# Kernel tuning notes

Measured on AMD Instinct MI355X. Metric: run time of the kernel, lower is better.

Reference implementation:

```python
import jax, jax.numpy as jnp
import numpy as np

C = 512

def _xavier(key, shape, gain=1.0):
    fan_in, fan_out = shape[1], shape[0]
    a = gain * np.sqrt(6.0 / (fan_in + fan_out))
    return jax.random.uniform(key, shape, jnp.float32, -a, a)

def setup_inputs() -> dict:
    key = jax.random.key(0)
    ks = jax.random.split(key, 5)
    x = jax.random.normal(ks[0], (32, C, 32, 32), jnp.float32)
    # 1x1 conv weights as [out_ch, in_ch]; biases zero-init per module
    Wq = _xavier(ks[1], (C, C))
    Wk = _xavier(ks[2], (C, C))
    Wv = _xavier(ks[3], (C, C))
    Wo = _xavier(ks[4], (C, C), gain=1e-05)
    zeros = jnp.zeros((C,), jnp.float32)
    return {"x": x, "Wq": Wq, "bq": zeros, "Wk": Wk, "bk": zeros,
            "Wv": Wv, "bv": zeros, "Wo": Wo, "bo": zeros}

def _proj(x, W, b):
    # 1x1 conv: x [B,C,H,W], W [Cout,Cin] -> [B,Cout,H,W]
    return jnp.einsum('bchw,oc->bohw', x, W) + b[None, :, None, None]

def reference(x, Wq, bq, Wk, bk, Wv, bv, Wo, bo):
    B, Cc, H, W = x.shape
    q = _proj(x, Wq, bq).transpose(0, 2, 3, 1).reshape(B, H * W, Cc)  # [B,HW,C]
    k = _proj(x, Wk, bk).reshape(B, Cc, H * W)                        # [B,C,HW]
    v = _proj(x, Wv, bv).transpose(0, 2, 3, 1).reshape(B, H * W, Cc)  # [B,HW,C]
    w = jnp.einsum('bnc,bcm->bnm', q, k) * (Cc ** -0.5)               # [B,HW,HW]
    w = jax.nn.softmax(w, axis=-1)
    h = jnp.einsum('bnm,bmc->bnc', w, v)                              # [B,HW,C]
    h = h.reshape(B, H, W, Cc).transpose(0, 3, 1, 2)                  # [B,C,H,W]
    h = _proj(h, Wo, bo)
    return x + h
```

## Files before the change

### kernel.cpp

```cpp
#include <hip/hip_runtime.h>
#include <stdint.h>


#define CD 512
#define NSP 1024
#define SCALE_EXP2 0.06376339f
#define WO_SCALE 4194304.0f
#define WO_INV   2.384185791015625e-7f

using bf16x8 = __attribute__((ext_vector_type(8))) short;
using f32x4  = __attribute__((ext_vector_type(4))) float;
typedef long i64v;

__device__ __forceinline__ unsigned char f2f8(float f) {
    unsigned int r;
    asm("v_cvt_pk_fp8_f32 %0, %1, %1" : "=v"(r) : "v"(f));
    return (unsigned char)(r & 0xffu);
}
__device__ __forceinline__ unsigned int f4_to_f8x4(float a, float b, float c, float d) {
    unsigned int r = 0;
    asm("v_cvt_pk_fp8_f32 %0, %2, %3\n\t"
        "v_cvt_pk_fp8_f32 %0, %4, %5 op_sel:[0,0,1]"
        : "=v"(r) : "0"(r), "v"(a), "v"(b), "v"(c), "v"(d));
    return r;
}
__device__ __forceinline__ void gl_lds16(const void* g, void* l) {
    __builtin_amdgcn_global_load_lds(
        (const __attribute__((address_space(1))) void*)g,
        (__attribute__((address_space(3))) void*)l, 16, 0, 0);
}

__global__ __launch_bounds__(256) void cvt_all(
    const float* __restrict__ Wq, const float* __restrict__ Wk,
    const float* __restrict__ Wv, const float* __restrict__ Wo,
    const float* __restrict__ bq, const float* __restrict__ bk,
    unsigned char* __restrict__ w8, float* __restrict__ bqk)
{
    int idx = blockIdx.x * 256 + threadIdx.x;
    int which = idx >> 18, off = idx & 262143;
    const float* src = which == 0 ? Wq : which == 1 ? Wk : which == 2 ? Wv : Wo;
    float v = src[off] * (which == 3 ? WO_SCALE : 1.0f);
    w8[idx] = f2f8(v);
    if (idx < 1024) bqk[idx] = (idx < 512) ? bq[idx] : bk[idx - 512];
}

__global__ __launch_bounds__(256) void transpose_x(const float* __restrict__ x,
                                                   unsigned char* __restrict__ xt) {
    __shared__ float t[32][33];
    int b = blockIdx.z;
    int n0 = blockIdx.x * 32, c0 = blockIdx.y * 32;
    const float* xb = x + (size_t)b * CD * NSP;
    unsigned char* xtb = xt + (size_t)b * NSP * CD;
    int tx = threadIdx.x, ty = threadIdx.y;
    #pragma unroll
    for (int i = 0; i < 4; ++i)
        t[ty + i * 8][tx] = xb[(size_t)(c0 + ty + i * 8) * NSP + n0 + tx];
    __syncthreads();
    #pragma unroll
    for (int i = 0; i < 4; ++i)
        xtb[(size_t)(n0 + ty + i * 8) * CD + c0 + tx] = f2f8(t[tx][ty + i * 8]);
}

template<int BIAS_MODE, bool RESID, bool OUT_F32>
__global__ __launch_bounds__(256)
void gemm_bt8(const unsigned char* __restrict__ A,
              const unsigned char* __restrict__ B,
              void* __restrict__ Cv,
              const float* __restrict__ bias,
              const float* __restrict__ resid,
              int K, int lda, int ldb, int ldc,
              long sA, long sB, long sC, long sR, float alpha)
{
    __shared__ __align__(16) unsigned char As[2][128 * 64];
    __shared__ __align__(16) unsigned char Bs[2][128 * 64];

    const int z = blockIdx.z;
    const unsigned char* Ab = A + (size_t)z * sA + (size_t)blockIdx.y * 128 * lda;
    const unsigned char* Bb = B + (size_t)z * sB + (size_t)blockIdx.x * 128 * ldb;

    const int t = threadIdx.x;
    const int lane = t & 63;
    const int wave = t >> 6;
    const int wr = wave >> 1, wc = wave & 1;
    const int lr = lane & 15, lk = lane >> 4;

    f32x4 acc[4][4] = {};

    const int KT = K >> 6;
    auto stage = [&](int kt, int buf) {
        int k0 = kt << 6;
        #pragma unroll
        for (int i = 0; i < 2; ++i) {
            int rb = i * 64 + wave * 16;
            int row = rb + (lane >> 2);
            int src = (lane & 3) ^ ((row >> 1) & 3);
            gl_lds16(Ab + (size_t)row * lda + k0 + src * 16, &As[buf][rb * 64]);
            gl_lds16(Bb + (size_t)row * ldb + k0 + src * 16, &Bs[buf][rb * 64]);
        }
    };
    stage(0, 0);
    for (int kt = 0; kt < KT; ++kt) {
        int cur = kt & 1;
        if (kt + 1 < KT) {
            stage(kt + 1, cur ^ 1);
            asm volatile("s_waitcnt vmcnt(4)" ::: "memory");
        } else {
            asm volatile("s_waitcnt vmcnt(0)" ::: "memory");
        }
        __builtin_amdgcn_s_barrier();
        const unsigned char* Ac = &As[cur][0];
        const unsigned char* Bc = &Bs[cur][0];
        #pragma unroll
        for (int kk = 0; kk < 2; ++kk) {
            int c16 = kk * 2 + (lk >> 1);
            int half = (lk & 1) * 8;
            i64v af[4], bfr[4];
            #pragma unroll
            for (int f = 0; f < 4; ++f) {
                int arow = wr * 64 + f * 16 + lr;
                af[f] = *(const i64v*)&Ac[arow * 64 + ((c16 ^ ((arow >> 1) & 3)) << 4) + half];
                int brow = wc * 64 + f * 16 + lr;
                bfr[f] = *(const i64v*)&Bc[brow * 64 + ((c16 ^ ((brow >> 1) & 3)) << 4) + half];
            }
            #pragma unroll
            for (int fm = 0; fm < 4; ++fm)
                #pragma unroll
                for (int fn = 0; fn < 4; ++fn)
                    acc[fm][fn] = __builtin_amdgcn_mfma_f32_16x16x32_fp8_fp8(
                        af[fm], bfr[fn], acc[fm][fn], 0, 0, 0);
        }
        asm volatile("s_waitcnt lgkmcnt(0)" ::: "memory");
        __builtin_amdgcn_s_barrier();
    }

    const int m0 = blockIdx.y * 128;
    const int n0 = blockIdx.x * 128;
    unsigned char* C8 = (unsigned char*)Cv + (size_t)z * sC;
    float* Cf = (float*)Cv + (size_t)z * sC;
    const float* rp = RESID ? resid + (size_t)z * sR : nullptr;
    #pragma unroll
    for (int fm = 0; fm < 4; ++fm) {
        #pragma unroll
        for (int fn = 0; fn < 4; ++fn) {
            int col = n0 + wc * 64 + fn * 16 + lr;
            int rowb = m0 + wr * 64 + fm * 16 + lk * 4;
            #pragma unroll
            for (int j = 0; j < 4; ++j) {
                int row = rowb + j;
                float v = acc[fm][fn][j] * alpha;
                if (BIAS_MODE == 1) v += bias[col];
                if (BIAS_MODE == 2) v += bias[row];
                if (RESID) v += rp[(size_t)row * ldc + col];
                if (OUT_F32) Cf[(size_t)row * ldc + col] = v;
                else         C8[(size_t)row * ldc + col] = f2f8(v);
            }
        }
    }
}

__global__ __launch_bounds__(512, 2)
void flash_attn(const unsigned char* __restrict__ Q,
                const unsigned char* __restrict__ Kg,
                const unsigned char* __restrict__ Vg,
                unsigned char* __restrict__ H)
{
    __shared__ __align__(16) unsigned char Ks[2][64 * 512];
    __shared__ __align__(16) unsigned char Vs[2][512 * 64];
    __shared__ __align__(16) unsigned char Ps[2][128 * 72];
    __shared__ __align__(16) float Ls[2][128];
    __shared__ int flags[2];

    const int p = blockIdx.x;
    const int b  = ((p >> 6) << 3) + (p & 7);
    const int qt = (p >> 3) & 7;

    const int tid = threadIdx.x;
    const int w = tid >> 6, lane = tid & 63;
    const int lr = lane & 15, lk = lane >> 4;
    const int q0 = qt * 128 + w * 16;

    i64v qf[16];
    const unsigned char* qp = Q + ((size_t)b * NSP + q0 + lr) * 1024 + lk * 8;
    #pragma unroll
    for (int st = 0; st < 16; ++st) qf[st] = *(const i64v*)(qp + st * 32);

    f32x4 o[8][4] = {};
    float m = -3.0e38f, l = 0.f;

    const unsigned char* Kb = Kg + (size_t)b * NSP * 1024;
    const unsigned char* Vb = Vg + (size_t)b * CD * 1024;

    auto stageK = [&](int t, int buf) {
        int kv0 = t * 64;
        #pragma unroll
        for (int i = 0; i < 4; ++i) {
            int rb = i * 16 + w * 2;
            int row = rb + (lane >> 5);
            int src = (lane & 31) ^ (row & 7);
            gl_lds16(Kb + (size_t)(kv0 + row) * 1024 + src * 16, &Ks[buf][rb * 512]);
        }
    };
    auto stageV = [&](int t, int buf) {
        int kv0 = t * 64;
        #pragma unroll
        for (int i = 0; i < 4; ++i) {
            int cb = i * 128 + w * 16;
            int c = cb + (lane >> 2);
            int src = (lane & 3) ^ ((c >> 1) & 3);
            gl_lds16(Vb + (size_t)c * 1024 + kv0 + src * 16, &Vs[buf][cb * 64]);
        }
    };

    auto qksm = [&](int tau) {
        const int pb = tau & 1;
        const unsigned char* Kc = &Ks[pb][0];
        f32x4 s[4] = {};
        __builtin_amdgcn_s_setprio(1);
        #pragma unroll
        for (int st = 0; st < 16; ++st) {
            int c16 = st * 2 + (lk >> 1);
            int half = (lk & 1) * 8;
            #pragma unroll
            for (int kvf = 0; kvf < 4; ++kvf) {
                int row = kvf * 16 + lr;
                i64v kf = *(const i64v*)&Kc[row * 512 + ((c16 ^ (row & 7)) << 4) + half];
                s[kvf] = __builtin_amdgcn_mfma_f32_16x16x32_fp8_fp8(kf, qf[st], s[kvf], 0, 0, 0);
            }
        }
        __builtin_amdgcn_s_setprio(0);
        #pragma unroll
        for (int kvf = 0; kvf < 4; ++kvf)
            #pragma unroll
            for (int j = 0; j < 4; ++j) s[kvf][j] *= SCALE_EXP2;

        float pm = fmaxf(fmaxf(fmaxf(s[0][0], s[0][1]), fmaxf(s[0][2], s[0][3])),
                         fmaxf(fmaxf(s[1][0], s[1][1]), fmaxf(s[1][2], s[1][3])));
        pm = fmaxf(pm, fmaxf(fmaxf(fmaxf(s[2][0], s[2][1]), fmaxf(s[2][2], s[2][3])),
                             fmaxf(fmaxf(s[3][0], s[3][1]), fmaxf(s[3][2], s[3][3]))));
        pm = fmaxf(pm, __shfl_xor(pm, 16));
        pm = fmaxf(pm, __shfl_xor(pm, 32));
        bool ev = !__all(pm - m <= 8.0f);
        float mn = fmaxf(m, pm);
        float sc = ev ? exp2f(m - mn) : 1.0f;
        if (ev) { m = mn; l *= sc; }
        if (lk == 0) Ls[pb][w * 16 + lr] = sc;
        if (ev && lane == 0) flags[pb] = tau;

        float rs = 0.f;
        #pragma unroll
        for (int kvf = 0; kvf < 4; ++kvf)
            #pragma unroll
            for (int j = 0; j < 4; ++j) {
                s[kvf][j] = exp2f(s[kvf][j] - m);
                rs += s[kvf][j];
            }
        rs += __shfl_xor(rs, 16);
        rs += __shfl_xor(rs, 32);
        l += rs;

        #pragma unroll
        for (int kvf = 0; kvf < 4; ++kvf) {
            unsigned int pk = f4_to_f8x4(s[kvf][0], s[kvf][1], s[kvf][2], s[kvf][3]);
            *(unsigned int*)&Ps[pb][(w * 16 + lr) * 72 + kvf * 16 + lk * 4] = pk;
        }
    };

    if (tid == 0) { flags[0] = -1; flags[1] = -1; }
    stageK(0, 0); stageV(0, 0);
    asm volatile("s_waitcnt vmcnt(0) lgkmcnt(0)" ::: "memory");
    __builtin_amdgcn_s_barrier();
    stageK(1, 1);
    qksm(0);
    asm volatile("s_waitcnt vmcnt(0) lgkmcnt(0)" ::: "memory");
    __builtin_amdgcn_s_barrier();

    for (int t = 0; t < 16; ++t) {
        const int cur = t & 1;
        if (t < 14) stageK(t + 2, cur);
        if (t < 15) stageV(t + 1, cur ^ 1);

        if (flags[cur] == t) {
            #pragma unroll
            for (int qf2 = 0; qf2 < 8; ++qf2) {
                f32x4 scv = *(const f32x4*)&Ls[cur][qf2 * 16 + lk * 4];
                #pragma unroll
                for (int cf = 0; cf < 4; ++cf) {
                    o[qf2][cf][0] *= scv[0]; o[qf2][cf][1] *= scv[1];
                    o[qf2][cf][2] *= scv[2]; o[qf2][cf][3] *= scv[3];
                }
            }
        }
        const unsigned char* Vc = &Vs[cur][0];
        __builtin_amdgcn_s_setprio(1);
        #pragma unroll
        for (int ks = 0; ks < 2; ++ks) {
            int c16 = ks * 2 + (lk >> 1);
            int half = (lk & 1) * 8;
            i64v vfr[4];
            #pragma unroll
            for (int cf = 0; cf < 4; ++cf) {
                int c = w * 64 + cf * 16 + lr;
                vfr[cf] = *(const i64v*)&Vc[c * 64 + ((c16 ^ ((c >> 1) & 3)) << 4) + half];
            }
            #pragma unroll
            for (int qf2 = 0; qf2 < 8; ++qf2) {
                i64v pa = *(const i64v*)&Ps[cur][(qf2 * 16 + lr) * 72 + ks * 32 + lk * 8];
                #pragma unroll
                for (int cf = 0; cf < 4; ++cf)
                    o[qf2][cf] = __builtin_amdgcn_mfma_f32_16x16x32_fp8_fp8(
                        pa, vfr[cf], o[qf2][cf], 0, 0, 0);
            }
        }
        __builtin_amdgcn_s_setprio(0);

        if (t < 15) qksm(t + 1);

        asm volatile("s_waitcnt vmcnt(0) lgkmcnt(0)" ::: "memory");
        __builtin_amdgcn_s_barrier();
    }

    if (lk == 0) Ls[0][w * 16 + lr] = 1.0f / l;
    asm volatile("s_waitcnt lgkmcnt(0)" ::: "memory");
    __builtin_amdgcn_s_barrier();
    unsigned char* Hp = H + ((size_t)b * NSP + qt * 128) * CD + w * 64;
    #pragma unroll
    for (int qf2 = 0; qf2 < 8; ++qf2) {
        f32x4 li = *(const f32x4*)&Ls[0][qf2 * 16 + lk * 4];
        #pragma unroll
        for (int cf = 0; cf < 4; ++cf) {
            #pragma unroll
            for (int j = 0; j < 4; ++j)
                Hp[(size_t)(qf2 * 16 + lk * 4 + j) * CD + cf * 16 + lr] =
                    f2f8(o[qf2][cf][j] * li[j]);
        }
    }
}

extern "C" void kernel_launch(void* const* d_in, const int* in_sizes, int n_in,
                              void* d_out, int out_size, void* d_ws, size_t ws_size,
                              hipStream_t stream)
{
    const float* x  = (const float*)d_in[0];
    const float* Wq = (const float*)d_in[1];
    const float* bq = (const float*)d_in[2];
    const float* Wk = (const float*)d_in[3];
    const float* bk = (const float*)d_in[4];
    const float* Wv = (const float*)d_in[5];
    const float* bv = (const float*)d_in[6];
    const float* Wo = (const float*)d_in[7];
    const float* bo = (const float*)d_in[8];
    float* out = (float*)d_out;

    unsigned char* w = (unsigned char*)d_ws;
    unsigned char* W8  = w;
    float*         bqk = (float*)(w + 1048576);
    unsigned char* Xt8 = w + 1052672;
    unsigned char* QK8 = w + 17829888;
    unsigned char* Vc8 = w + 51384320;
    unsigned char* H8  = w + 68161536;

    cvt_all<<<4096, 256, 0, stream>>>(Wq, Wk, Wv, Wo, bq, bk, W8, bqk);
    transpose_x<<<dim3(32, 16, 32), dim3(32, 8), 0, stream>>>(x, Xt8);

    gemm_bt8<1, false, false><<<dim3(8, 256, 1), 256, 0, stream>>>(
        Xt8, W8, QK8, bqk, nullptr, 512, 512, 512, 1024, 0, 0, 0, 0, 1.0f);

    gemm_bt8<2, false, false><<<dim3(8, 4, 32), 256, 0, stream>>>(
        W8 + 524288, Xt8, Vc8, bv, nullptr, 512, 512, 512, 1024,
        0, 524288, 524288, 0, 1.0f);

    flash_attn<<<256, 512, 0, stream>>>(QK8, QK8 + 512, Vc8, H8);

    gemm_bt8<2, true, true><<<dim3(8, 4, 32), 256, 0, stream>>>(
        W8 + 786432, H8, out, bo, x, 512, 512, 512, 1024,
        0, 524288, 524288, 524288, WO_INV);
}
```

Baseline: 196.9 us.

## Interleave QK and PV MFMAs in flash attention; enlarge projection GEMM tiles

The flash attention loop now issues the PV MFMAs for tile t and the QK^T MFMAs for tile t+1 in one interleaved loop, followed by softmax. The aim is to overlap LDS fragment loads with MFMA work and shorten the dependency chain. The last iteration is peeled out. Separately, the QKV projection GEMMs move to a 256x128 tile with 4x8 fragments per wave, which improves operand reuse but raises register pressure and halves the block count.

```diff
diff --git a/kernel.cpp b/kernel.cpp
--- a/kernel.cpp
+++ b/kernel.cpp
@@ -8,7 +8,6 @@
 #define WO_SCALE 4194304.0f
 #define WO_INV   2.384185791015625e-7f
 
-using bf16x8 = __attribute__((ext_vector_type(8))) short;
 using f32x4  = __attribute__((ext_vector_type(4))) float;
 typedef long i64v;
 
@@ -61,21 +60,120 @@
         xtb[(size_t)(n0 + ty + i * 8) * CD + c0 + tx] = f2f8(t[tx][ty + i * 8]);
 }
 
-template<int BIAS_MODE, bool RESID, bool OUT_F32>
+template<int BIAS_MODE>
 __global__ __launch_bounds__(256)
-void gemm_bt8(const unsigned char* __restrict__ A,
-              const unsigned char* __restrict__ B,
-              void* __restrict__ Cv,
-              const float* __restrict__ bias,
-              const float* __restrict__ resid,
-              int K, int lda, int ldb, int ldc,
-              long sA, long sB, long sC, long sR, float alpha)
+void gemm_bt8_256(const unsigned char* __restrict__ A,
+                  const unsigned char* __restrict__ B,
+                  unsigned char* __restrict__ C8,
+                  const float* __restrict__ bias,
+                  int K, int lda, int ldb, int ldc,
+                  long sA, long sB, long sC)
+{
+    __shared__ __align__(16) unsigned char As[2][256 * 64];
+    __shared__ __align__(16) unsigned char Bs[2][128 * 64];
+
+    const int z = blockIdx.z;
+    const unsigned char* Ab = A + (size_t)z * sA + (size_t)blockIdx.y * 256 * lda;
+    const unsigned char* Bb = B + (size_t)z * sB + (size_t)blockIdx.x * 128 * ldb;
+
+    const int t = threadIdx.x;
+    const int lane = t & 63;
+    const int wave = t >> 6;
+    const int lr = lane & 15, lk = lane >> 4;
+
+    f32x4 acc[4][8] = {};
+
+    const int KT = K >> 6;
+    auto stage = [&](int kt, int buf) {
+        int k0 = kt << 6;
+        #pragma unroll
+        for (int i = 0; i < 4; ++i) {
+            int rb = i * 64 + wave * 16;
+            int row = rb + (lane >> 2);
+            int src = (lane & 3) ^ ((row >> 1) & 3);
+            gl_lds16(Ab + (size_t)row * lda + k0 + src * 16, &As[buf][rb * 64]);
+        }
+        #pragma unroll
+        for (int i = 0; i < 2; ++i) {
+            int rb = i * 64 + wave * 16;
+            int row = rb + (lane >> 2);
+            int src = (lane & 3) ^ ((row >> 1) & 3);
+            gl_lds16(Bb + (size_t)row * ldb + k0 + src * 16, &Bs[buf][rb * 64]);
+        }
+    };
+    stage(0, 0);
+    for (int kt = 0; kt < KT; ++kt) {
+        int cur = kt & 1;
+        if (kt + 1 < KT) {
+            stage(kt + 1, cur ^ 1);
+            asm volatile("s_waitcnt vmcnt(6)" ::: "memory");
+        } else {
+            asm volatile("s_waitcnt vmcnt(0)" ::: "memory");
+        }
+        __builtin_amdgcn_s_barrier();
+        const unsigned char* Ac = &As[cur][0];
+        const unsigned char* Bc = &Bs[cur][0];
+        #pragma unroll
+        for (int kk = 0; kk < 2; ++kk) {
+            int c16 = kk * 2 + (lk >> 1);
+            int half = (lk & 1) * 8;
+            i64v af[4], bfr[8];
+            #pragma unroll
+            for (int f = 0; f < 4; ++f) {
+                int arow = wave * 64 + f * 16 + lr;
+                af[f] = *(const i64v*)&Ac[arow * 64 + ((c16 ^ ((arow >> 1) & 3)) << 4) + half];
+            }
+            #pragma unroll
+            for (int fn = 0; fn < 8; ++fn) {
+                int brow = fn * 16 + lr;
+                bfr[fn] = *(const i64v*)&Bc[brow * 64 + ((c16 ^ ((brow >> 1) & 3)) << 4) + half];
+            }
+            #pragma unroll
+            for (int fm = 0; fm < 4; ++fm)
+                #pragma unroll
+                for (int fn = 0; fn < 8; ++fn)
+                    acc[fm][fn] = __builtin_amdgcn_mfma_f32_16x16x32_fp8_fp8(
+                        af[fm], bfr[fn], acc[fm][fn], 0, 0, 0);
+        }
+        asm volatile("s_waitcnt lgkmcnt(0)" ::: "memory");
+        __builtin_amdgcn_s_barrier();
+    }
+
+    const int m0 = blockIdx.y * 256;
+    const int n0 = blockIdx.x * 128;
+    unsigned char* Cp = C8 + (size_t)z * sC;
+    #pragma unroll
+    for (int fm = 0; fm < 4; ++fm) {
+        #pragma unroll
+        for (int fn = 0; fn < 8; ++fn) {
+            int col = n0 + fn * 16 + lr;
+            int rowb = m0 + wave * 64 + fm * 16 + lk * 4;
+            #pragma unroll
+            for (int j = 0; j < 4; ++j) {
+                int row = rowb + j;
+                float v = acc[fm][fn][j];
+                if (BIAS_MODE == 1) v += bias[col];
+                if (BIAS_MODE == 2) v += bias[row];
+                Cp[(size_t)row * ldc + col] = f2f8(v);
+            }
+        }
+    }
+}
+
+__global__ __launch_bounds__(256)
+void gemm_bt8_out(const unsigned char* __restrict__ A,
+                  const unsigned char* __restrict__ B,
+                  float* __restrict__ Cf,
+                  const float* __restrict__ bias,
+                  const float* __restrict__ resid,
+                  int K, int lda, int ldb, int ldc,
+                  long sB, long sC, long sR, float alpha)
 {
     __shared__ __align__(16) unsigned char As[2][128 * 64];
     __shared__ __align__(16) unsigned char Bs[2][128 * 64];
 
     const int z = blockIdx.z;
-    const unsigned char* Ab = A + (size_t)z * sA + (size_t)blockIdx.y * 128 * lda;
+    const unsigned char* Ab = A + (size_t)blockIdx.y * 128 * lda;
     const unsigned char* Bb = B + (size_t)z * sB + (size_t)blockIdx.x * 128 * ldb;
 
     const int t = threadIdx.x;
@@ -135,9 +233,8 @@
 
     const int m0 = blockIdx.y * 128;
     const int n0 = blockIdx.x * 128;
-    unsigned char* C8 = (unsigned char*)Cv + (size_t)z * sC;
-    float* Cf = (float*)Cv + (size_t)z * sC;
-    const float* rp = RESID ? resid + (size_t)z * sR : nullptr;
+    float* Co = Cf + (size_t)z * sC;
+    const float* rp = resid + (size_t)z * sR;
     #pragma unroll
     for (int fm = 0; fm < 4; ++fm) {
         #pragma unroll
@@ -147,12 +244,8 @@
             #pragma unroll
             for (int j = 0; j < 4; ++j) {
                 int row = rowb + j;
-                float v = acc[fm][fn][j] * alpha;
-                if (BIAS_MODE == 1) v += bias[col];
-                if (BIAS_MODE == 2) v += bias[row];
-                if (RESID) v += rp[(size_t)row * ldc + col];
-                if (OUT_F32) Cf[(size_t)row * ldc + col] = v;
-                else         C8[(size_t)row * ldc + col] = f2f8(v);
+                Co[(size_t)row * ldc + col] = acc[fm][fn][j] * alpha
+                    + bias[row] + rp[(size_t)row * ldc + col];
             }
         }
     }
@@ -211,28 +304,12 @@
         }
     };
 
-    auto qksm = [&](int tau) {
+    auto softmax_pack = [&](int tau, f32x4* s) {
         const int pb = tau & 1;
-        const unsigned char* Kc = &Ks[pb][0];
-        f32x4 s[4] = {};
-        __builtin_amdgcn_s_setprio(1);
-        #pragma unroll
-        for (int st = 0; st < 16; ++st) {
-            int c16 = st * 2 + (lk >> 1);
-            int half = (lk & 1) * 8;
-            #pragma unroll
-            for (int kvf = 0; kvf < 4; ++kvf) {
-                int row = kvf * 16 + lr;
-                i64v kf = *(const i64v*)&Kc[row * 512 + ((c16 ^ (row & 7)) << 4) + half];
-                s[kvf] = __builtin_amdgcn_mfma_f32_16x16x32_fp8_fp8(kf, qf[st], s[kvf], 0, 0, 0);
-            }
-        }
-        __builtin_amdgcn_s_setprio(0);
         #pragma unroll
         for (int kvf = 0; kvf < 4; ++kvf)
             #pragma unroll
             for (int j = 0; j < 4; ++j) s[kvf][j] *= SCALE_EXP2;
-
         float pm = fmaxf(fmaxf(fmaxf(s[0][0], s[0][1]), fmaxf(s[0][2], s[0][3])),
                          fmaxf(fmaxf(s[1][0], s[1][1]), fmaxf(s[1][2], s[1][3])));
         pm = fmaxf(pm, fmaxf(fmaxf(fmaxf(s[2][0], s[2][1]), fmaxf(s[2][2], s[2][3])),
@@ -245,7 +322,6 @@
         if (ev) { m = mn; l *= sc; }
         if (lk == 0) Ls[pb][w * 16 + lr] = sc;
         if (ev && lane == 0) flags[pb] = tau;
-
         float rs = 0.f;
         #pragma unroll
         for (int kvf = 0; kvf < 4; ++kvf)
@@ -257,11 +333,22 @@
         rs += __shfl_xor(rs, 16);
         rs += __shfl_xor(rs, 32);
         l += rs;
-
         #pragma unroll
         for (int kvf = 0; kvf < 4; ++kvf) {
             unsigned int pk = f4_to_f8x4(s[kvf][0], s[kvf][1], s[kvf][2], s[kvf][3]);
             *(unsigned int*)&Ps[pb][(w * 16 + lr) * 72 + kvf * 16 + lk * 4] = pk;
+        }
+    };
+
+    auto rescale_o = [&](int pb) {
+        #pragma unroll
+        for (int qf2 = 0; qf2 < 8; ++qf2) {
+            f32x4 scv = *(const f32x4*)&Ls[pb][qf2 * 16 + lk * 4];
+            #pragma unroll
+            for (int cf = 0; cf < 4; ++cf) {
+                o[qf2][cf][0] *= scv[0]; o[qf2][cf][1] *= scv[1];
+                o[qf2][cf][2] *= scv[2]; o[qf2][cf][3] *= scv[3];
+            }
         }
     };
 
@@ -270,27 +357,81 @@
     asm volatile("s_waitcnt vmcnt(0) lgkmcnt(0)" ::: "memory");
     __builtin_amdgcn_s_barrier();
     stageK(1, 1);
-    qksm(0);
+    {
+        f32x4 s[4] = {};
+        const unsigned char* Kc = &Ks[0][0];
+        #pragma unroll
+        for (int st = 0; st < 16; ++st) {
+            int c16 = st * 2 + (lk >> 1);
+            int half = (lk & 1) * 8;
+            #pragma unroll
+            for (int kvf = 0; kvf < 4; ++kvf) {
+                int row = kvf * 16 + lr;
+                i64v kf = *(const i64v*)&Kc[row * 512 + ((c16 ^ (row & 7)) << 4) + half];
+                s[kvf] = __builtin_amdgcn_mfma_f32_16x16x32_fp8_fp8(kf, qf[st], s[kvf], 0, 0, 0);
+            }
+        }
+        softmax_pack(0, s);
+    }
     asm volatile("s_waitcnt vmcnt(0) lgkmcnt(0)" ::: "memory");
     __builtin_amdgcn_s_barrier();
 
-    for (int t = 0; t < 16; ++t) {
+    for (int t = 0; t < 15; ++t) {
         const int cur = t & 1;
         if (t < 14) stageK(t + 2, cur);
-        if (t < 15) stageV(t + 1, cur ^ 1);
-
-        if (flags[cur] == t) {
-            #pragma unroll
-            for (int qf2 = 0; qf2 < 8; ++qf2) {
-                f32x4 scv = *(const f32x4*)&Ls[cur][qf2 * 16 + lk * 4];
+        stageV(t + 1, cur ^ 1);
+        if (flags[cur] == t) rescale_o(cur);
+
+        const unsigned char* Vc = &Vs[cur][0];
+        const unsigned char* Pc = &Ps[cur][0];
+        const unsigned char* Kc = &Ks[cur ^ 1][0];
+        f32x4 s[4] = {};
+        i64v vfr[4];
+        __builtin_amdgcn_s_setprio(1);
+        #pragma unroll
+        for (int st = 0; st < 16; ++st) {
+            const int ks = st >> 3;
+            const int qf2 = st & 7;
+            if ((st & 7) == 0) {
+                int c16v = ks * 2 + (lk >> 1);
+                int halfv = (lk & 1) * 8;
                 #pragma unroll
                 for (int cf = 0; cf < 4; ++cf) {
-                    o[qf2][cf][0] *= scv[0]; o[qf2][cf][1] *= scv[1];
-                    o[qf2][cf][2] *= scv[2]; o[qf2][cf][3] *= scv[3];
+                    int c = w * 64 + cf * 16 + lr;
+                    vfr[cf] = *(const i64v*)&Vc[c * 64 + ((c16v ^ ((c >> 1) & 3)) << 4) + halfv];
                 }
             }
-        }
+            i64v pa = *(const i64v*)&Pc[(qf2 * 16 + lr) * 72 + ks * 32 + lk * 8];
+            int c16 = st * 2 + (lk >> 1);
+            int half = (lk & 1) * 8;
+            i64v kf[4];
+            #pragma unroll
+            for (int kvf = 0; kvf < 4; ++kvf) {
+                int row = kvf * 16 + lr;
+                kf[kvf] = *(const i64v*)&Kc[row * 512 + ((c16 ^ (row & 7)) << 4) + half];
+            }
+            #pragma unroll
+            for (int cf = 0; cf < 4; ++cf)
+                o[qf2][cf] = __builtin_amdgcn_mfma_f32_16x16x32_fp8_fp8(
+                    pa, vfr[cf], o[qf2][cf], 0, 0, 0);
+            #pragma unroll
+            for (int kvf = 0; kvf < 4; ++kvf)
+                s[kvf] = __builtin_amdgcn_mfma_f32_16x16x32_fp8_fp8(
+                    kf[kvf], qf[st], s[kvf], 0, 0, 0);
+        }
+        __builtin_amdgcn_s_setprio(0);
+
+        softmax_pack(t + 1, s);
+
+        asm volatile("s_waitcnt vmcnt(0) lgkmcnt(0)" ::: "memory");
+        __builtin_amdgcn_s_barrier();
+    }
+
+    {
+        const int cur = 1;
+        if (flags[cur] == 15) rescale_o(cur);
         const unsigned char* Vc = &Vs[cur][0];
+        const unsigned char* Pc = &Ps[cur][0];
         __builtin_amdgcn_s_setprio(1);
         #pragma unroll
         for (int ks = 0; ks < 2; ++ks) {
@@ -304,7 +445,7 @@
             }
             #pragma unroll
             for (int qf2 = 0; qf2 < 8; ++qf2) {
-                i64v pa = *(const i64v*)&Ps[cur][(qf2 * 16 + lr) * 72 + ks * 32 + lk * 8];
+                i64v pa = *(const i64v*)&Pc[(qf2 * 16 + lr) * 72 + ks * 32 + lk * 8];
                 #pragma unroll
                 for (int cf = 0; cf < 4; ++cf)
                     o[qf2][cf] = __builtin_amdgcn_mfma_f32_16x16x32_fp8_fp8(
@@ -312,10 +453,7 @@
             }
         }
         __builtin_amdgcn_s_setprio(0);
-
-        if (t < 15) qksm(t + 1);
-
-        asm volatile("s_waitcnt vmcnt(0) lgkmcnt(0)" ::: "memory");
+        asm volatile("s_waitcnt lgkmcnt(0)" ::: "memory");
         __builtin_amdgcn_s_barrier();
     }
 
@@ -362,16 +500,15 @@
     cvt_all<<<4096, 256, 0, stream>>>(Wq, Wk, Wv, Wo, bq, bk, W8, bqk);
     transpose_x<<<dim3(32, 16, 32), dim3(32, 8), 0, stream>>>(x, Xt8);
 
-    gemm_bt8<1, false, false><<<dim3(8, 256, 1), 256, 0, stream>>>(
-        Xt8, W8, QK8, bqk, nullptr, 512, 512, 512, 1024, 0, 0, 0, 0, 1.0f);
-
-    gemm_bt8<2, false, false><<<dim3(8, 4, 32), 256, 0, stream>>>(
-        W8 + 524288, Xt8, Vc8, bv, nullptr, 512, 512, 512, 1024,
-        0, 524288, 524288, 0, 1.0f);
+    gemm_bt8_256<1><<<dim3(8, 128, 1), 256, 0, stream>>>(
+        Xt8, W8, QK8, bqk, 512, 512, 512, 1024, 0, 0, 0);
+
+    gemm_bt8_256<2><<<dim3(8, 2, 32), 256, 0, stream>>>(
+        W8 + 524288, Xt8, Vc8, bv, 512, 512, 512, 1024, 0, 524288, 524288);
 
     flash_attn<<<256, 512, 0, stream>>>(QK8, QK8 + 512, Vc8, H8);
 
-    gemm_bt8<2, true, true><<<dim3(8, 4, 32), 256, 0, stream>>>(
+    gemm_bt8_out<<<dim3(8, 4, 32), 256, 0, stream>>>(
         W8 + 786432, H8, out, bo, x, 512, 512, 512, 1024,
-        0, 524288, 524288, 524288, WO_INV);
-}
+        524288, 524288, 524288, WO_INV);
+}
```

Result: slower. 232.0 us (+17.8%).
